# Performance work log

Hardware: AMD Instinct MI355X
Metric: run time of the kernel (lower is better)

Reference implementation:

```python
import jax, jax.numpy as jnp
import numpy as np

EPS = 1e-5

def _conv3x3(x, w, stride=1):
    # x: [N,C,H,W], w: [O,I,3,3], padding=1
    return jax.lax.conv_general_dilated(
        x, w,
        window_strides=(stride, stride),
        padding=((1, 1), (1, 1)),
        dimension_numbers=("NCHW", "OIHW", "NCHW"),
    )

def _bn(x, gamma, beta, mean, var):
    # inference-mode BatchNorm2d with running stats; per-channel over C of NCHW
    inv = gamma * jax.lax.rsqrt(var + EPS)
    return x * inv[None, :, None, None] + (beta - mean * inv)[None, :, None, None]

def setup_inputs() -> dict:
    key = jax.random.key(0)
    ks = jax.random.split(key, 11)
    N, C, H, W = 32, 256, 56, 56
    x = jax.random.normal(ks[0], (N, C, H, W), dtype=jnp.float32)
    fan = C * 9
    w1 = jax.random.normal(ks[1], (C, C, 3, 3), dtype=jnp.float32) / np.sqrt(fan)
    w2 = jax.random.normal(ks[2], (C, C, 3, 3), dtype=jnp.float32) / np.sqrt(fan)
    g1 = jax.random.uniform(ks[3], (C,), dtype=jnp.float32, minval=0.5, maxval=1.5)
    b1 = jax.random.normal(ks[4], (C,), dtype=jnp.float32) * 0.1
    m1 = jax.random.normal(ks[5], (C,), dtype=jnp.float32) * 0.1
    v1 = jax.random.uniform(ks[6], (C,), dtype=jnp.float32, minval=0.5, maxval=1.5)
    g2 = jax.random.uniform(ks[7], (C,), dtype=jnp.float32, minval=0.5, maxval=1.5)
    b2 = jax.random.normal(ks[8], (C,), dtype=jnp.float32) * 0.1
    m2 = jax.random.normal(ks[9], (C,), dtype=jnp.float32) * 0.1
    v2 = jax.random.uniform(ks[10], (C,), dtype=jnp.float32, minval=0.5, maxval=1.5)
    return {"x": x, "w1": w1, "g1": g1, "b1": b1, "m1": m1, "v1": v1,
            "w2": w2, "g2": g2, "b2": b2, "m2": m2, "v2": v2}

def reference(x, w1, g1, b1, m1, v1, w2, g2, b2, m2, v2):
    identity = x
    out = jax.nn.relu(_bn(_conv3x3(x, w1, stride=1), g1, b1, m1, v1))
    out = _bn(_conv3x3(out, w2, stride=1), g2, b2, m2, v2)
    return jax.nn.relu(out + identity)
```

## Files before the change

kernel.cpp:

```cpp
#include <hip/hip_runtime.h>
#include <hip/hip_bf16.h>


typedef __attribute__((ext_vector_type(8))) short bf16x8;
typedef __attribute__((ext_vector_type(4))) float f32x4;
typedef __attribute__((ext_vector_type(4))) unsigned int uint4v;

#define C_CH   256
#define HW_IMG 3136
#define CHW    802816
#define WELEM  589824
#define WROWS  192
#define RSTR   40
#define BUFE   7680
#define NCH    8
#define NSTEP  72

__device__ __forceinline__ ushort f2bf(float f){
    union{__hip_bfloat16 h; ushort u;} c; c.h = __float2bfloat16(f); return c.u;
}

__global__ __launch_bounds__(256) void prep_kernel(
    const float* __restrict__ w1, const float* __restrict__ w2,
    const float* __restrict__ g1, const float* __restrict__ b1,
    const float* __restrict__ m1, const float* __restrict__ v1,
    const float* __restrict__ g2, const float* __restrict__ b2,
    const float* __restrict__ m2, const float* __restrict__ v2,
    ushort* __restrict__ wf1, ushort* __restrict__ wf2,
    float* __restrict__ bn, ushort* __restrict__ zb)
{
    int gid = blockIdx.x * 256 + threadIdx.x;
    if (gid < WELEM) {
        int j = gid & 7, l = (gid >> 3) & 63, ct = (gid >> 9) & 15, rr = gid >> 13;
        int c = rr / 9, r = rr - c * 9;
        int co = ct * 16 + (l & 15);
        int ci = c * 32 + (l >> 4) * 8 + j;
        wf1[gid] = f2bf(w1[(co * C_CH + ci) * 9 + r]);
    }
    int g2i = gid - WELEM;
    if (g2i >= 0 && g2i < WELEM) {
        int j = g2i & 7, l = (g2i >> 3) & 63, ct = (g2i >> 9) & 15, rr = g2i >> 13;
        int c = rr / 9, r = rr - c * 9;
        int co = ct * 16 + (l & 15);
        int ci = c * 32 + (l >> 4) * 8 + j;
        wf2[g2i] = f2bf(w2[(co * C_CH + ci) * 9 + r]);
    }
    if (gid < C_CH) {
        float i1 = g1[gid] * rsqrtf(v1[gid] + 1e-5f);
        bn[gid]            = i1;
        bn[C_CH + gid]     = b1[gid] - m1[gid] * i1;
        float i2 = g2[gid] * rsqrtf(v2[gid] + 1e-5f);
        bn[2*C_CH + gid]   = i2;
        bn[3*C_CH + gid]   = b2[gid] - m2[gid] * i2;
    }
    if (gid < 512) zb[gid] = 0;
}

__global__ __launch_bounds__(256) void xpose_kernel(
    const float* __restrict__ x, ushort* __restrict__ xT)
{
    __shared__ ushort T[64 * 72];
    int tid = threadIdx.x;
    int b = blockIdx.x;
    int n = b / 196, rem = b % 196;
    int pb = rem >> 2, cb = rem & 3;
    int lane = tid & 63, cr = tid >> 6;
    const float* xp = x + ((size_t)(n * C_CH + cb * 64)) * HW_IMG + pb * 64 + lane;
#pragma unroll
    for (int j = 0; j < 16; ++j) {
        int cil = cr * 16 + j;
        T[lane * 72 + cil] = f2bf(xp[(size_t)cil * HW_IMG]);
    }
    __syncthreads();
#pragma unroll
    for (int it = 0; it < 2; ++it) {
        int slot = it * 256 + tid;
        int p = slot >> 3, g = slot & 7;
        uint4v v = *(const uint4v*)&T[p * 72 + g * 8];
        *(uint4v*)(xT + ((size_t)n * HW_IMG + pb * 64 + p) * C_CH + cb * 64 + g * 8) = v;
    }
}

template<bool SECOND>
__global__ __launch_bounds__(256, 3) void conv_kernel(
    const ushort* __restrict__ srcT,
    const ushort* __restrict__ wf,
    const float* __restrict__ bnp,
    const float* __restrict__ ident,
    const ushort* __restrict__ zb,
    void* __restrict__ dst)
{
    __shared__ ushort B[16896];

    const int tid = threadIdx.x;
    const int wv = tid >> 6, l = tid & 63;
    const int lr = l & 15, lg = l >> 4;

    int bid = blockIdx.x;
    int swz = (bid & 7) * 196 + (bid >> 3);
    const int n = swz / 49, pt = swz % 49;
    const int p0 = pt * 64;

    bool wLa[4], wRa[4];
    int vbe[4];
#pragma unroll
    for (int nc = 0; nc < 4; ++nc) {
        int p = p0 + nc * 16 + lr;
        int w = p % 56;
        wLa[nc] = (w > 0);
        wRa[nc] = (w < 55);
        vbe[nc] = (64 + nc * 16 + lr) * RSTR + lg * 8;
    }

    const ushort* sA[4];
#pragma unroll
    for (int rd = 0; rd < 4; ++rd) {
        int slot = rd * 256 + tid;
        int row = slot / 5, g = slot - row * 5;
        int gp = p0 - 64 + row;
        bool val = (g < 4) && (gp >= 0) && (gp < HW_IMG) && (slot < 960);
        sA[rd] = val ? (srcT + ((size_t)n * HW_IMG + gp) * C_CH + g * 8)
                     : (zb + g * 8);
    }

    auto stage = [&](int cix, int bufE) {
#pragma unroll
        for (int rd = 0; rd < 4; ++rd) {
            if (rd < 3 || tid < 192) {
                __builtin_amdgcn_global_load_lds(
                    (const __attribute__((address_space(1))) void*)(sA[rd] + cix * 32),
                    (__attribute__((address_space(3))) void*)&B[bufE + (rd * 256 + tid) * 8],
                    16, 0, 0);
            }
        }
    };

    f32x4 acc[4][4];
#pragma unroll
    for (int mr = 0; mr < 4; ++mr)
#pragma unroll
        for (int nc = 0; nc < 4; ++nc) {
            f32x4 z = {0.f, 0.f, 0.f, 0.f};
            acc[mr][nc] = z;
        }
    const bf16x8 z8 = {0,0,0,0,0,0,0,0};

    bf16x8 areg[3][4];
    const ushort* pWb = wf + wv * 2048 + l * 8;

    auto loadA = [&](int t, bf16x8* a) {
#pragma unroll
        for (int mr = 0; mr < 4; ++mr)
            a[mr] = *(const bf16x8*)(pWb + t * 8192 + mr * 512);
    };

    stage(0, 0);
    loadA(0, areg[0]);
    loadA(1, areg[1]);
    __syncthreads();

#pragma unroll
    for (int c = 0; c < NCH; ++c) {
        const int bufE = (c & 1) ? BUFE : 0;
#pragma unroll
        for (int s = 0; s < 9; ++s) {
            const int t = c * 9 + s;
            if (t + 2 < NSTEP) loadA(t + 2, areg[(t + 2) % 3]);
            if (s == 3 && c + 1 < NCH) stage(c + 1, bufE ^ BUFE);
            const int dh = s / 3 - 1, dw = s % 3 - 1;
            const int off = dh * 56 + dw;
            bf16x8 bq[4];
#pragma unroll
            for (int nc = 0; nc < 4; ++nc) {
                bq[nc] = *(const bf16x8*)&B[vbe[nc] + bufE + off * RSTR];
                if (dw == -1) bq[nc] = wLa[nc] ? bq[nc] : z8;
                if (dw ==  1) bq[nc] = wRa[nc] ? bq[nc] : z8;
            }
            __builtin_amdgcn_s_setprio(1);
#pragma unroll
            for (int mr = 0; mr < 4; ++mr)
#pragma unroll
                for (int nc = 0; nc < 4; ++nc)
                    acc[mr][nc] = __builtin_amdgcn_mfma_f32_16x16x32_bf16(
                        areg[t % 3][mr], bq[nc], acc[mr][nc], 0, 0, 0);
            __builtin_amdgcn_s_setprio(0);
        }
        __syncthreads();
    }

    if constexpr (!SECOND) {
        ushort* T = B;
#pragma unroll
        for (int mr = 0; mr < 4; ++mr) {
#pragma unroll
            for (int nc = 0; nc < 4; ++nc) {
                int co0 = wv * 64 + mr * 16 + lg * 4;
                float v0 = fmaxf(acc[mr][nc][0] * bnp[co0+0] + bnp[C_CH+co0+0], 0.f);
                float v1 = fmaxf(acc[mr][nc][1] * bnp[co0+1] + bnp[C_CH+co0+1], 0.f);
                float v2 = fmaxf(acc[mr][nc][2] * bnp[co0+2] + bnp[C_CH+co0+2], 0.f);
                float v3 = fmaxf(acc[mr][nc][3] * bnp[co0+3] + bnp[C_CH+co0+3], 0.f);
                uint2 pk;
                pk.x = (uint)f2bf(v0) | ((uint)f2bf(v1) << 16);
                pk.y = (uint)f2bf(v2) | ((uint)f2bf(v3) << 16);
                *(uint2*)&T[(nc * 16 + lr) * 264 + co0] = pk;
            }
        }
        __syncthreads();
        ushort* yT = (ushort*)dst;
#pragma unroll
        for (int it = 0; it < 8; ++it) {
            int slot = it * 256 + tid;
            int row = slot >> 5, g = slot & 31;
            uint4v v = *(const uint4v*)&T[row * 264 + g * 8];
            *(uint4v*)(yT + ((size_t)n * HW_IMG + p0 + row) * C_CH + g * 8) = v;
        }
    } else {
        const size_t nbase = (size_t)n * CHW;
        float* out = (float*)dst;
#pragma unroll
        for (int mr = 0; mr < 4; ++mr) {
#pragma unroll
            for (int nc = 0; nc < 4; ++nc) {
                int pc = p0 + nc * 16 + lr;
#pragma unroll
                for (int i = 0; i < 4; ++i) {
                    int co = wv * 64 + mr * 16 + lg * 4 + i;
                    size_t o = nbase + (size_t)co * HW_IMG + pc;
                    float val = acc[mr][nc][i] * bnp[co] + bnp[C_CH + co] + ident[o];
                    out[o] = fmaxf(val, 0.f);
                }
            }
        }
    }
}

extern "C" void kernel_launch(void* const* d_in, const int* in_sizes, int n_in,
                              void* d_out, int out_size, void* d_ws, size_t ws_size,
                              hipStream_t stream) {
    const float* x  = (const float*)d_in[0];
    const float* w1 = (const float*)d_in[1];
    const float* g1 = (const float*)d_in[2];
    const float* b1 = (const float*)d_in[3];
    const float* m1 = (const float*)d_in[4];
    const float* v1 = (const float*)d_in[5];
    const float* w2 = (const float*)d_in[6];
    const float* g2 = (const float*)d_in[7];
    const float* b2 = (const float*)d_in[8];
    const float* m2 = (const float*)d_in[9];
    const float* v2 = (const float*)d_in[10];

    ushort* wf1 = (ushort*)d_ws;
    ushort* wf2 = wf1 + WELEM;
    float*  bn  = (float*)(wf2 + WELEM);
    ushort* zb  = (ushort*)(bn + 4 * C_CH);
    ushort* yT  = zb + 512;
    ushort* xT  = (ushort*)d_out;

    prep_kernel<<<dim3(4608), dim3(256), 0, stream>>>(
        w1, w2, g1, b1, m1, v1, g2, b2, m2, v2, wf1, wf2, bn, zb);

    xpose_kernel<<<dim3(6272), dim3(256), 0, stream>>>(x, xT);

    conv_kernel<false><<<dim3(1568), dim3(256), 0, stream>>>(
        xT, wf1, bn, x, zb, (void*)yT);

    conv_kernel<true><<<dim3(1568), dim3(256), 0, stream>>>(
        yT, wf2, bn + 512, x, zb, d_out);
}
```

Measured before the change: 263.2 us.

## Software-pipeline LDS B-fragment reads in half-steps and mask borders via zero row

Each tap step is split into two half-steps of two column tiles, and the B fragments for the next half-step are read from LDS before the current MFMAs run, so LDS latency overlaps matrix math. Border masking now redirects out-of-range reads to a zeroed LDS row instead of selecting after the load, which removes per-element select instructions. The cost is extra registers for the double-buffered fragments and a small zero-initialised LDS region.

```diff
diff --git a/kernel.cpp b/kernel.cpp
--- a/kernel.cpp
+++ b/kernel.cpp
@@ -15,6 +15,7 @@
 #define BUFE   7680
 #define NCH    8
 #define NSTEP  72
+#define ZROW   15360
 
 __device__ __forceinline__ ushort f2bf(float f){
     union{__hip_bfloat16 h; ushort u;} c; c.h = __float2bfloat16(f); return c.u;
@@ -111,6 +112,7 @@
         wRa[nc] = (w < 55);
         vbe[nc] = (64 + nc * 16 + lr) * RSTR + lg * 8;
     }
+    const int zidx = ZROW + lg * 8;
 
     const ushort* sA[4];
 #pragma unroll
@@ -143,7 +145,6 @@
             f32x4 z = {0.f, 0.f, 0.f, 0.f};
             acc[mr][nc] = z;
         }
-    const bf16x8 z8 = {0,0,0,0,0,0,0,0};
 
     bf16x8 areg[3][4];
     const ushort* pWb = wf + wv * 2048 + l * 8;
@@ -154,7 +155,21 @@
             a[mr] = *(const bf16x8*)(pWb + t * 8192 + mr * 512);
     };
 
+    auto readB = [&](int bufE, int ht, bf16x8* dstq) {
+        const int s = ht >> 1, q = ht & 1;
+        const int dw = s % 3 - 1;
+        const int off = (s / 3 - 1) * 56 * RSTR + dw * RSTR + bufE;
+#pragma unroll
+        for (int i = 0; i < 2; ++i) {
+            int nc = q * 2 + i;
+            bool ok = (dw == -1) ? wLa[nc] : ((dw == 1) ? wRa[nc] : true);
+            int idx = ok ? (vbe[nc] + off) : zidx;
+            dstq[i] = *(const bf16x8*)&B[idx];
+        }
+    };
+
     stage(0, 0);
+    if (tid < 40) B[ZROW + tid] = 0;
     loadA(0, areg[0]);
     loadA(1, areg[1]);
     __syncthreads();
@@ -162,27 +177,23 @@
 #pragma unroll
     for (int c = 0; c < NCH; ++c) {
         const int bufE = (c & 1) ? BUFE : 0;
-#pragma unroll
-        for (int s = 0; s < 9; ++s) {
+        bf16x8 bq0[2], bq1[2];
+        readB(bufE, 0, bq0);
+#pragma unroll
+        for (int ht = 0; ht < 18; ++ht) {
+            const int s = ht >> 1, q = ht & 1;
             const int t = c * 9 + s;
-            if (t + 2 < NSTEP) loadA(t + 2, areg[(t + 2) % 3]);
-            if (s == 3 && c + 1 < NCH) stage(c + 1, bufE ^ BUFE);
-            const int dh = s / 3 - 1, dw = s % 3 - 1;
-            const int off = dh * 56 + dw;
-            bf16x8 bq[4];
-#pragma unroll
-            for (int nc = 0; nc < 4; ++nc) {
-                bq[nc] = *(const bf16x8*)&B[vbe[nc] + bufE + off * RSTR];
-                if (dw == -1) bq[nc] = wLa[nc] ? bq[nc] : z8;
-                if (dw ==  1) bq[nc] = wRa[nc] ? bq[nc] : z8;
-            }
+            if (q == 0 && t + 2 < NSTEP) loadA(t + 2, areg[(t + 2) % 3]);
+            if (ht == 6 && c + 1 < NCH) stage(c + 1, bufE ^ BUFE);
+            if (ht + 1 < 18) readB(bufE, ht + 1, (ht & 1) ? bq0 : bq1);
+            bf16x8* bq = (ht & 1) ? bq1 : bq0;
             __builtin_amdgcn_s_setprio(1);
 #pragma unroll
             for (int mr = 0; mr < 4; ++mr)
 #pragma unroll
-                for (int nc = 0; nc < 4; ++nc)
-                    acc[mr][nc] = __builtin_amdgcn_mfma_f32_16x16x32_bf16(
-                        areg[t % 3][mr], bq[nc], acc[mr][nc], 0, 0, 0);
+                for (int i = 0; i < 2; ++i)
+                    acc[mr][q * 2 + i] = __builtin_amdgcn_mfma_f32_16x16x32_bf16(
+                        areg[t % 3][mr], bq[i], acc[mr][q * 2 + i], 0, 0, 0);
             __builtin_amdgcn_s_setprio(0);
         }
         __syncthreads();
```

Measured after the change: 374.8 us. 42.4% more time.
